# Kernel tuning notes

Measured on AMD Instinct MI355X. Metric: run time of the kernel, lower is better.

Reference implementation:

```python
import jax, jax.numpy as jnp
import numpy as np

EPS = 1e-5
K = 16  # neighbors

def bn(x, g, b):
    # BatchNorm in training mode: stats over all axes except the last (channel)
    ax = tuple(range(x.ndim - 1))
    m = x.mean(ax, keepdims=True)
    v = x.var(ax, keepdims=True)
    return g * (x - m) * jax.lax.rsqrt(v + EPS) + b

def setup_inputs() -> dict:
    key = jax.random.key(0)
    ks = jax.random.split(key, 12)
    B, N, M, C, D = 2, 16384, 4096, 32, 64
    H = D // 2
    p = lambda k, s: jax.random.normal(k, s, dtype=jnp.float32) * 0.1
    inp = {}
    inp["xyz"] = jax.random.normal(ks[0], (B, N, 3), dtype=jnp.float32)
    inp["feats"] = jax.random.normal(ks[1], (B, C, N), dtype=jnp.float32)
    inp["sample_idx"] = jax.random.randint(ks[2], (B, M), 0, N, dtype=jnp.int32)
    # RelativePosEncoder mlp: Conv2d(10, H, 1) + BN
    inp["W_pos"] = p(ks[3], (10, H)); inp["b_pos"] = jnp.zeros(H); inp["g_pos"] = jnp.ones(H); inp["be_pos"] = jnp.zeros(H)
    # feature_mlp: Conv2d(C, H, 1) + BN
    inp["W_feat"] = p(ks[4], (C, H)); inp["b_feat"] = jnp.zeros(H); inp["g_feat"] = jnp.ones(H); inp["be_feat"] = jnp.zeros(H)
    # attention score mlp: Conv2d(D, D, 1, bias=False)
    inp["W_score"] = p(ks[5], (D, D))
    # out_mlp: Conv1d(D, D, 1, bias=False) + BN
    inp["W_out"] = p(ks[6], (D, D)); inp["g_out"] = jnp.ones(D); inp["be_out"] = jnp.zeros(D)
    # LFA shortcut: Conv1d(C, D, 1, bias=False) + BN
    inp["W_sc1"] = p(ks[7], (C, D)); inp["g_sc1"] = jnp.ones(D); inp["be_sc1"] = jnp.zeros(D)
    # unit shortcut: Conv1d(C, D, 1, bias=False) + BN
    inp["W_sc2"] = p(ks[8], (C, D)); inp["g_sc2"] = jnp.ones(D); inp["be_sc2"] = jnp.zeros(D)
    return inp

def reference(xyz, feats, sample_idx,
              W_pos, b_pos, g_pos, be_pos,
              W_feat, b_feat, g_feat, be_feat,
              W_score,
              W_out, g_out, be_out,
              W_sc1, g_sc1, be_sc1,
              W_sc2, g_sc2, be_sc2):
    B, C, N = feats.shape
    featsT = jnp.transpose(feats, (0, 2, 1))                    # [B,N,C]
    xyz_ds = jnp.take_along_axis(xyz, sample_idx[:, :, None], axis=1)  # [B,M,3]
    # KNN: squared distances are monotone in cdist -> same topk indices
    d2 = jnp.sum((xyz_ds[:, :, None, :] - xyz[:, None, :, :]) ** 2, axis=-1)  # [B,M,N]
    _, knn_idx = jax.lax.top_k(-d2, K)                           # [B,M,K]
    gather = jax.vmap(lambda pts, idx: pts[idx])
    neigh_xyz = gather(xyz, knn_idx)                             # [B,M,K,3]
    neigh_feats = gather(featsT, knn_idx)                        # [B,M,K,C]
    center_feats = jnp.take_along_axis(featsT, sample_idx[:, :, None], axis=1)  # [B,M,C]
    # relative position encoding
    center = jnp.broadcast_to(xyz_ds[:, :, None, :], neigh_xyz.shape)
    rel = xyz_ds[:, :, None, :] - neigh_xyz                      # [B,M,K,3]
    dist = jnp.linalg.norm(rel, axis=-1, keepdims=True)          # [B,M,K,1]
    posf = jnp.concatenate([center, neigh_xyz, rel, dist], axis=-1)  # [B,M,K,10]
    pos_feats = jax.nn.relu(bn(posf @ W_pos + b_pos, g_pos, be_pos))       # [B,M,K,H]
    feat_feats = jax.nn.relu(bn(neigh_feats @ W_feat + b_feat, g_feat, be_feat))  # [B,M,K,H]
    combined = jnp.concatenate([feat_feats, pos_feats], axis=-1)  # [B,M,K,D]
    # attention pooling: softmax over the K (neighbor) axis
    scores = jax.nn.softmax(combined @ W_score, axis=2)
    pooled = jnp.sum(scores * combined, axis=2)                  # [B,M,D]
    out = jax.nn.relu(bn(pooled @ W_out, g_out, be_out))         # [B,M,D]
    sc1 = bn(jnp.mean(neigh_feats, axis=2) @ W_sc1, g_sc1, be_sc1)
    f_lfa = out + sc1
    f_sc = bn(center_feats @ W_sc2, g_sc2, be_sc2)
    y = jax.nn.relu(f_lfa + f_sc)                                # [B,M,D]
    return xyz_ds, jnp.transpose(y, (0, 2, 1)), sample_idx
```

## Files before the change

### kernel.cpp

```cpp
#include <hip/hip_runtime.h>
#include <math.h>

#define BB 2
#define NN 16384
#define MM 4096
#define C_IN 32
#define D_DIM 64
#define H_DIM 32
#define KNB 16
#define EPSV 1e-5f
#define FLT_BIG 3.0e38f
#define CAPK 128
#define NSPL 4
#define SPTS (NN / NSPL)

#define SPOS_SUM 0
#define SPOS_SQ 32
#define SFEAT_SUM 64
#define SFEAT_SQ 96
#define SSC1_SUM 128
#define SSC1_SQ 192
#define SSC2_SUM 256
#define SSC2_SQ 320
#define SOUT_SUM 384
#define SOUT_SQ 448
#define STATS_LEN 512
#define PA_W 384
#define PB_W 128
#define NBLK (BB * MM / 4)

__device__ __forceinline__ int clampi_r14(int v, int lo, int hi) {
    return v < lo ? lo : (v > hi ? hi : v);
}

__global__ __launch_bounds__(256) void prep_r14(const float* __restrict__ feats,
                                                const float* __restrict__ xyz,
                                                const int* __restrict__ sample_idx,
                                                float* __restrict__ featsT,
                                                float* __restrict__ xyz4,
                                                float* __restrict__ stats,
                                                float* __restrict__ out) {
    __shared__ float tile[C_IN][65];
    const int tid = threadIdx.x;
    const int b = blockIdx.x >> 8;
    const int n0 = (blockIdx.x & 255) * 64;
#pragma unroll
    for (int it = 0; it < 8; ++it) {
        int c = (tid >> 6) + 4 * it;
        int n = tid & 63;
        tile[c][n] = feats[((size_t)b * C_IN + c) * NN + n0 + n];
    }
    int e = blockIdx.x * 256 + tid;
    if (e < STATS_LEN) stats[e] = 0.f;
    if (e < BB * NN) {
        float x = xyz[e * 3 + 0], y = xyz[e * 3 + 1], z = xyz[e * 3 + 2];
        xyz4[e * 4 + 0] = x;
        xyz4[e * 4 + 1] = y;
        xyz4[e * 4 + 2] = z;
        xyz4[e * 4 + 3] = x * x + y * y + z * z;
    }
    if (e < BB * MM) {
        int bb2 = e >> 12;
        int sidx = clampi_r14(sample_idx[e], 0, NN - 1);
        const float* p = xyz + (size_t)(bb2 * NN + sidx) * 3;
        out[e * 3 + 0] = p[0];
        out[e * 3 + 1] = p[1];
        out[e * 3 + 2] = p[2];
        out[BB * MM * 3 + BB * D_DIM * MM + e] = (float)sample_idx[e];
    }
    __syncthreads();
#pragma unroll
    for (int it = 0; it < 8; ++it) {
        int c = tid & 31;
        int nn = (tid >> 5) + 8 * it;
        featsT[((size_t)b * NN + n0 + nn) * C_IN + c] = tile[c][nn];
    }
}

__device__ void knn_fullsplit_r14(const float* __restrict__ base4, int n0,
                                  float m2x, float m2y, float m2z, int lane,
                                  float* __restrict__ outd, int* __restrict__ outi) {
    float d2v[KNB]; int iv[KNB];
#pragma unroll
    for (int i = 0; i < KNB; i++) { d2v[i] = FLT_BIG; iv[i] = 0x7FFFFFFF; }
    float curmax = FLT_BIG; int amax = 0;
    for (int t = 0; t < SPTS / 64; ++t) {
        int n = n0 + lane + t * 64;
        const float4 p = *reinterpret_cast<const float4*>(base4 + (size_t)n * 4);
        float d2 = fmaf(p.x, m2x, p.w);
        d2 = fmaf(p.y, m2y, d2);
        d2 = fmaf(p.z, m2z, d2);
        if (d2 < curmax) {
#pragma unroll
            for (int i = 0; i < KNB; i++)
                if (i == amax) { d2v[i] = d2; iv[i] = n; }
            curmax = d2v[0]; amax = 0;
#pragma unroll
            for (int i = 1; i < KNB; i++)
                if (d2v[i] > curmax) { curmax = d2v[i]; amax = i; }
        }
    }
#pragma unroll
    for (int i = 0; i < KNB; i++) {
#pragma unroll
        for (int j = 0; j < KNB - 1; j++) {
            bool sw = (d2v[j] > d2v[j + 1]) ||
                      (d2v[j] == d2v[j + 1] && iv[j] > iv[j + 1]);
            if (sw) {
                float td = d2v[j]; d2v[j] = d2v[j + 1]; d2v[j + 1] = td;
                int   ti = iv[j];  iv[j]  = iv[j + 1];  iv[j + 1]  = ti;
            }
        }
    }
    float myd = FLT_BIG; int myidx = 0x7FFFFFFF;
#pragma unroll 1
    for (int r = 0; r < KNB; r++) {
        float cv = d2v[0]; int cid = iv[0]; int ml = lane;
#pragma unroll
        for (int off = 32; off > 0; off >>= 1) {
            float ov = __shfl_xor(cv, off);
            int   oid = __shfl_xor(cid, off);
            int   ol = __shfl_xor(ml, off);
            bool take = (ov < cv) || (ov == cv && oid < cid);
            cv = take ? ov : cv; cid = take ? oid : cid; ml = take ? ol : ml;
        }
        if (lane == r) { myd = cv; myidx = cid; }
        if (lane == ml) {
#pragma unroll
            for (int i = 0; i < KNB - 1; i++) { d2v[i] = d2v[i + 1]; iv[i] = iv[i + 1]; }
            d2v[KNB - 1] = FLT_BIG; iv[KNB - 1] = 0x7FFFFFFF;
        }
    }
    if (lane < KNB) { outd[lane] = myd; outi[lane] = myidx; }
}

__global__ __launch_bounds__(256) void knn_r14(const float* __restrict__ xyz4,
                                               const int* __restrict__ sample_idx,
                                               float* __restrict__ cand_d,
                                               int* __restrict__ cand_i) {
    __shared__ float bufd[16][CAPK];
    __shared__ int   bufi[16][CAPK];
    __shared__ int   cnt_lds[16];
    const int tid = threadIdx.x;
    const int w = tid >> 6, lane = tid & 63;
    const int split = blockIdx.x & (NSPL - 1);
    const int qgrp = blockIdx.x >> 2;
    const int qbase = qgrp * 16 + w * 4;
    const int b = qbase >> 12;
    const int n0 = split * SPTS;
    if (tid < 16) cnt_lds[tid] = 0;
    __syncthreads();
    const float* base4 = xyz4 + (size_t)b * NN * 4;
    const float4* p4 = reinterpret_cast<const float4*>(base4) + n0 + lane;

    float m2x[4], m2y[4], m2z[4], md[4], v16[4];
#pragma unroll
    for (int j = 0; j < 4; j++) {
        int s = clampi_r14(sample_idx[qbase + j], 0, NN - 1);
        m2x[j] = -2.f * base4[(size_t)s * 4 + 0];
        m2y[j] = -2.f * base4[(size_t)s * 4 + 1];
        m2z[j] = -2.f * base4[(size_t)s * 4 + 2];
        md[j] = FLT_BIG;
    }
#pragma unroll 8
    for (int it = 0; it < SPTS / 64; ++it) {
        const float4 p = p4[(size_t)it * 64];
#pragma unroll
        for (int j = 0; j < 4; j++) {
            float t = fmaf(p.x, m2x[j], p.w);
            t = fmaf(p.y, m2y[j], t);
            t = fmaf(p.z, m2z[j], t);
            md[j] = fminf(md[j], t);
        }
    }
#pragma unroll 1
    for (int j = 0; j < 4; j++) {
        unsigned fb = __float_as_uint(md[j]);
        unsigned key = (fb & 0x80000000u) ? ~fb : (fb | 0x80000000u);
        unsigned lo = 0u, hi = 0xFFFFFFFFu;
#pragma unroll 1
        for (int itb = 0; itb < 18; ++itb) {
            unsigned mid = lo + ((hi - lo) >> 1);
            unsigned long long bal = __ballot(key <= mid);
            int c = __popcll(bal);
            if (c >= KNB) hi = mid; else lo = mid + 1;
        }
        unsigned vb = (hi & 0x80000000u) ? (hi & 0x7FFFFFFFu) : ~hi;
        v16[j] = __uint_as_float(vb);
    }
#pragma unroll 4
    for (int it = 0; it < SPTS / 64; ++it) {
        const float4 p = p4[(size_t)it * 64];
        const int n = n0 + lane + it * 64;
#pragma unroll
        for (int j = 0; j < 4; j++) {
            float t = fmaf(p.x, m2x[j], p.w);
            t = fmaf(p.y, m2y[j], t);
            t = fmaf(p.z, m2z[j], t);
            if (t <= v16[j]) {
                int pos = atomicAdd(&cnt_lds[w * 4 + j], 1);
                if (pos < CAPK) { bufd[w * 4 + j][pos] = t; bufi[w * 4 + j][pos] = n; }
            }
        }
    }
    __threadfence_block();
#pragma unroll 1
    for (int j = 0; j < 4; j++) {
        const int qi = w * 4 + j;
        const int cnt = cnt_lds[qi];
        const int q = qbase + j;
        float* outd = cand_d + ((size_t)q * NSPL + split) * KNB;
        int*   outi = cand_i + ((size_t)q * NSPL + split) * KNB;
        if (cnt <= CAPK) {
#pragma unroll 1
            for (int half = 0; half < 2; ++half) {
                int i = lane + 64 * half;
                if (i < cnt) {
                    float di = bufd[qi][i]; int xi = bufi[qi][i];
                    int rank = 0;
                    for (int t = 0; t < cnt; ++t) {
                        float dt = bufd[qi][t]; int xt = bufi[qi][t];
                        rank += (dt < di || (dt == di && xt < xi)) ? 1 : 0;
                    }
                    if (rank < KNB) { outd[rank] = di; outi[rank] = xi; }
                }
            }
        } else {
            knn_fullsplit_r14(base4, n0, m2x[j], m2y[j], m2z[j], lane, outd, outi);
        }
    }
}

__device__ __forceinline__ void prebn_r14(const float (*posf)[12], const float (*nf)[C_IN],
                                          int k, int h,
                                          const float* __restrict__ W_pos, const float* __restrict__ b_pos,
                                          const float* __restrict__ W_feat, const float* __restrict__ b_feat,
                                          float* a_out, float* f_out) {
    float4 p0 = *reinterpret_cast<const float4*>(&posf[k][0]);
    float4 p1 = *reinterpret_cast<const float4*>(&posf[k][4]);
    float p8 = posf[k][8], p9 = posf[k][9];
    float a = b_pos[h];
    a += p0.x * W_pos[0 * H_DIM + h]; a += p0.y * W_pos[1 * H_DIM + h];
    a += p0.z * W_pos[2 * H_DIM + h]; a += p0.w * W_pos[3 * H_DIM + h];
    a += p1.x * W_pos[4 * H_DIM + h]; a += p1.y * W_pos[5 * H_DIM + h];
    a += p1.z * W_pos[6 * H_DIM + h]; a += p1.w * W_pos[7 * H_DIM + h];
    a += p8 * W_pos[8 * H_DIM + h];   a += p9 * W_pos[9 * H_DIM + h];
    float f = b_feat[h];
#pragma unroll
    for (int j4 = 0; j4 < C_IN / 4; ++j4) {
        float4 c = *reinterpret_cast<const float4*>(&nf[k][j4 * 4]);
        f += c.x * W_feat[(j4 * 4 + 0) * H_DIM + h];
        f += c.y * W_feat[(j4 * 4 + 1) * H_DIM + h];
        f += c.z * W_feat[(j4 * 4 + 2) * H_DIM + h];
        f += c.w * W_feat[(j4 * 4 + 3) * H_DIM + h];
    }
    *a_out = a; *f_out = f;
}

__global__ __launch_bounds__(256) void stageA_r14(const float* __restrict__ xyz4,
                                                  const int* __restrict__ sample_idx,
                                                  const float* __restrict__ featsT,
                                                  const float* __restrict__ cand_d,
                                                  const int* __restrict__ cand_i,
                                                  const float* __restrict__ W_pos, const float* __restrict__ b_pos,
                                                  const float* __restrict__ W_feat, const float* __restrict__ b_feat,
                                                  const float* __restrict__ W_sc1, const float* __restrict__ W_sc2,
                                                  float* __restrict__ combpre,
                                                  float* __restrict__ sc1_pre, float* __restrict__ sc2_pre,
                                                  float* __restrict__ partialsA) {
    __shared__ int   idxs[4][KNB];
    __shared__ float sd[4][64];
    __shared__ int   si[4][64];
    __shared__ __align__(16) float posf[4][KNB][12];
    __shared__ __align__(16) float nf[4][KNB][C_IN];
    __shared__ float meanf[4][C_IN];
    __shared__ float centerf[4][C_IN];
    __shared__ float posS[4][H_DIM], posQ[4][H_DIM], featS[4][H_DIM], featQ[4][H_DIM];
    __shared__ float s1S[4][D_DIM], s1Q[4][D_DIM], s2S[4][D_DIM], s2Q[4][D_DIM];
    const int tid = threadIdx.x;
    const int w = tid >> 6, lane = tid & 63;
    const int q = blockIdx.x * 4 + w;
    const int b = q >> 12;
    const int sidx = clampi_r14(sample_idx[q], 0, NN - 1);
    const float* base4 = xyz4 + (size_t)b * NN * 4;

    float d = cand_d[(size_t)q * 64 + lane];
    int   i = cand_i[(size_t)q * 64 + lane];
    float qx = base4[(size_t)sidx * 4 + 0];
    float qy = base4[(size_t)sidx * 4 + 1];
    float qz = base4[(size_t)sidx * 4 + 2];
    float cfv = 0.f;
    if (lane < C_IN) cfv = featsT[((size_t)b * NN + sidx) * C_IN + lane];

    {
        sd[w][lane] = d; si[w][lane] = i;
        __syncthreads();
        int rank = 0;
#pragma unroll
        for (int t = 0; t < 64; ++t) {
            float dt = sd[w][t]; int it = si[w][t];
            rank += (dt < d || (dt == d && it < i)) ? 1 : 0;
        }
        if (rank < KNB) idxs[w][rank] = i;
        if (lane < C_IN) centerf[w][lane] = cfv;
        __syncthreads();
    }

    if (lane < KNB) {
        int idx = clampi_r14(idxs[w][lane], 0, NN - 1);
        float nx = base4[(size_t)idx * 4 + 0];
        float ny = base4[(size_t)idx * 4 + 1];
        float nz = base4[(size_t)idx * 4 + 2];
        float rx = qx - nx, ry = qy - ny, rz = qz - nz;
        float dist = sqrtf(rx * rx + ry * ry + rz * rz);
        posf[w][lane][0] = qx; posf[w][lane][1] = qy; posf[w][lane][2] = qz;
        posf[w][lane][3] = nx; posf[w][lane][4] = ny; posf[w][lane][5] = nz;
        posf[w][lane][6] = rx; posf[w][lane][7] = ry; posf[w][lane][8] = rz;
        posf[w][lane][9] = dist; posf[w][lane][10] = 0.f; posf[w][lane][11] = 0.f;
    }
    __syncthreads();
    const float* fT = featsT + (size_t)b * NN * C_IN;
#pragma unroll
    for (int ii = 0; ii < 2; ++ii) {
        int e4 = lane + 64 * ii;
        int k = e4 >> 3, c4 = e4 & 7;
        const float4 v = *reinterpret_cast<const float4*>(fT + (size_t)idxs[w][k] * C_IN + c4 * 4);
        *reinterpret_cast<float4*>(&nf[w][k][c4 * 4]) = v;
    }
    __syncthreads();

    const int h = lane & 31;
    float sP = 0.f, qP = 0.f, sF = 0.f, qF = 0.f;
    float* cp = combpre + (size_t)q * (KNB * D_DIM);
#pragma unroll
    for (int i2 = 0; i2 < 8; i2++) {
        int k = ((lane + 64 * i2) >> 5);
        float a, f;
        prebn_r14(posf[w], nf[w], k, h, W_pos, b_pos, W_feat, b_feat, &a, &f);
        sP += a; qP += a * a;
        sF += f; qF += f * f;
        cp[k * D_DIM + h] = f;
        cp[k * D_DIM + H_DIM + h] = a;
    }
    sP += __shfl_xor(sP, 32); qP += __shfl_xor(qP, 32);
    sF += __shfl_xor(sF, 32); qF += __shfl_xor(qF, 32);
    if (lane < H_DIM) {
        posS[w][h] = sP; posQ[w][h] = qP; featS[w][h] = sF; featQ[w][h] = qF;
    }
    if (lane < C_IN) {
        float s = 0.f;
#pragma unroll
        for (int k = 0; k < KNB; k++) s += nf[w][k][lane];
        meanf[w][lane] = s * (1.f / (float)KNB);
    }
    __syncthreads();
    {
        float a = 0.f, c2 = 0.f;
#pragma unroll
        for (int j = 0; j < C_IN; j++) {
            a  += meanf[w][j]   * W_sc1[j * D_DIM + lane];
            c2 += centerf[w][j] * W_sc2[j * D_DIM + lane];
        }
        sc1_pre[(size_t)q * D_DIM + lane] = a;
        sc2_pre[(size_t)q * D_DIM + lane] = c2;
        s1S[w][lane] = a;  s1Q[w][lane] = a * a;
        s2S[w][lane] = c2; s2Q[w][lane] = c2 * c2;
    }
    __syncthreads();
    float* row = partialsA + (size_t)blockIdx.x * PA_W;
    if (tid < H_DIM) {
        row[SPOS_SUM + tid]  = posS[0][tid] + posS[1][tid] + posS[2][tid] + posS[3][tid];
        row[SPOS_SQ + tid]   = posQ[0][tid] + posQ[1][tid] + posQ[2][tid] + posQ[3][tid];
        row[SFEAT_SUM + tid] = featS[0][tid] + featS[1][tid] + featS[2][tid] + featS[3][tid];
        row[SFEAT_SQ + tid]  = featQ[0][tid] + featQ[1][tid] + featQ[2][tid] + featQ[3][tid];
    } else if (tid >= 64 && tid < 128) {
        int dd = tid - 64;
        row[SSC1_SUM + dd] = s1S[0][dd] + s1S[1][dd] + s1S[2][dd] + s1S[3][dd];
        row[SSC1_SQ + dd]  = s1Q[0][dd] + s1Q[1][dd] + s1Q[2][dd] + s1Q[3][dd];
    } else if (tid >= 128 && tid < 192) {
        int dd = tid - 128;
        row[SSC2_SUM + dd] = s2S[0][dd] + s2S[1][dd] + s2S[2][dd] + s2S[3][dd];
        row[SSC2_SQ + dd]  = s2Q[0][dd] + s2Q[1][dd] + s2Q[2][dd] + s2Q[3][dd];
    }
}

#define NRSPLIT 64
__global__ __launch_bounds__(256) void reduce_r14(const float* __restrict__ partials,
                                                  int rows, int width,
                                                  float* __restrict__ stats_out) {
    const int wchunks = (width + 255) / 256;
    const int wi = blockIdx.x % wchunks;
    const int pi = blockIdx.x / wchunks;
    const int c = wi * 256 + threadIdx.x;
    if (c >= width) return;
    const int per = rows / NRSPLIT;
    const int p0 = pi * per;
    float s = 0.f;
    for (int p = p0; p < p0 + per; ++p) s += partials[(size_t)p * width + c];
    atomicAdd(&stats_out[c], s);
}

__global__ __launch_bounds__(256) void stageB_r14(const float* __restrict__ combpre,
                                                  const float* __restrict__ g_pos, const float* __restrict__ be_pos,
                                                  const float* __restrict__ g_feat, const float* __restrict__ be_feat,
                                                  const float* __restrict__ W_score, const float* __restrict__ W_out,
                                                  const float* __restrict__ stats,
                                                  float* __restrict__ out_pre,
                                                  float* __restrict__ partialsB) {
    __shared__ __align__(16) float comb[4][KNB][D_DIM];
    __shared__ float scl[D_DIM], shf[D_DIM];
    __shared__ float pooled[4][D_DIM];
    __shared__ float oS[4][D_DIM], oQ[4][D_DIM];
    const int tid = threadIdx.x;
    const int w = tid >> 6, lane = tid & 63;
    const int q = blockIdx.x * 4 + w;

    if (tid < D_DIM) {
        const float inv1 = 1.f / (float)(BB * MM * KNB);
        float mean, var, g, bb;
        if (tid < H_DIM) {
            mean = stats[SFEAT_SUM + tid] * inv1;
            var  = fmaxf(stats[SFEAT_SQ + tid] * inv1 - mean * mean, 0.f);
            g = g_feat[tid]; bb = be_feat[tid];
        } else {
            int h = tid - H_DIM;
            mean = stats[SPOS_SUM + h] * inv1;
            var  = fmaxf(stats[SPOS_SQ + h] * inv1 - mean * mean, 0.f);
            g = g_pos[h]; bb = be_pos[h];
        }
        float s = g * rsqrtf(var + EPSV);
        scl[tid] = s;
        shf[tid] = bb - mean * s;
    }
    __syncthreads();

    const float4* src = reinterpret_cast<const float4*>(combpre + (size_t)blockIdx.x * 4 * KNB * D_DIM);
#pragma unroll
    for (int i = 0; i < 4; ++i) {
        int f = tid + 256 * i;
        int qloc = f >> 8;
        int k = (f >> 4) & 15;
        int j4 = f & 15;
        float4 v = src[f];
        int j = j4 * 4;
        v.x = fmaxf(v.x * scl[j + 0] + shf[j + 0], 0.f);
        v.y = fmaxf(v.y * scl[j + 1] + shf[j + 1], 0.f);
        v.z = fmaxf(v.z * scl[j + 2] + shf[j + 2], 0.f);
        v.w = fmaxf(v.w * scl[j + 3] + shf[j + 3], 0.f);
        *reinterpret_cast<float4*>(&comb[qloc][k][j]) = v;
    }
    __syncthreads();

    const int d = lane;
    float s[KNB];
#pragma unroll
    for (int k = 0; k < KNB; k++) s[k] = 0.f;
#pragma unroll 4
    for (int j4 = 0; j4 < D_DIM / 4; ++j4) {
        float w0 = W_score[(j4 * 4 + 0) * D_DIM + d];
        float w1 = W_score[(j4 * 4 + 1) * D_DIM + d];
        float w2 = W_score[(j4 * 4 + 2) * D_DIM + d];
        float w3 = W_score[(j4 * 4 + 3) * D_DIM + d];
#pragma unroll
        for (int k = 0; k < KNB; k++) {
            float4 cb = *reinterpret_cast<const float4*>(&comb[w][k][j4 * 4]);
            s[k] += cb.x * w0 + cb.y * w1 + cb.z * w2 + cb.w * w3;
        }
    }
    float mx = s[0];
#pragma unroll
    for (int k = 1; k < KNB; k++) mx = fmaxf(mx, s[k]);
    float sum = 0.f;
#pragma unroll
    for (int k = 0; k < KNB; k++) { s[k] = __expf(s[k] - mx); sum += s[k]; }
    float inv = 1.f / sum;
    float pv = 0.f;
#pragma unroll
    for (int k = 0; k < KNB; k++) pv += s[k] * inv * comb[w][k][d];
    pooled[w][d] = pv;
    __syncthreads();
    float o = 0.f;
#pragma unroll
    for (int dd = 0; dd < D_DIM; dd++) o += pooled[w][dd] * W_out[dd * D_DIM + d];
    out_pre[(size_t)q * D_DIM + d] = o;
    oS[w][d] = o; oQ[w][d] = o * o;
    __syncthreads();
    float* row = partialsB + (size_t)blockIdx.x * PB_W;
    if (tid < D_DIM) {
        row[tid] = oS[0][tid] + oS[1][tid] + oS[2][tid] + oS[3][tid];
    } else if (tid < 2 * D_DIM) {
        int dd = tid - D_DIM;
        row[D_DIM + dd] = oQ[0][dd] + oQ[1][dd] + oQ[2][dd] + oQ[3][dd];
    }
}

__global__ __launch_bounds__(256) void final_r14(const float* __restrict__ out_pre,
                                                 const float* __restrict__ sc1_pre,
                                                 const float* __restrict__ sc2_pre,
                                                 const float* __restrict__ stats,
                                                 const float* __restrict__ g_out, const float* __restrict__ be_out,
                                                 const float* __restrict__ g_sc1, const float* __restrict__ be_sc1,
                                                 const float* __restrict__ g_sc2, const float* __restrict__ be_sc2,
                                                 float* __restrict__ out) {
    __shared__ float yt[64][65];
    const int tid = threadIdx.x;
    const int blk = blockIdx.x;
    const int b = blk >> 6;
    const int m0 = (blk & 63) * 64;
    const int d = tid & 63;

    const float invn = 1.f / (float)(BB * MM);
    float mo = stats[SOUT_SUM + d] * invn;
    float vo = fmaxf(stats[SOUT_SQ + d] * invn - mo * mo, 0.f);
    float so = g_out[d] * rsqrtf(vo + EPSV);
    float oo = be_out[d] - mo * so;
    float m1 = stats[SSC1_SUM + d] * invn;
    float v1 = fmaxf(stats[SSC1_SQ + d] * invn - m1 * m1, 0.f);
    float s1 = g_sc1[d] * rsqrtf(v1 + EPSV);
    float o1 = be_sc1[d] - m1 * s1;
    float m2 = stats[SSC2_SUM + d] * invn;
    float v2 = fmaxf(stats[SSC2_SQ + d] * invn - m2 * m2, 0.f);
    float s2 = g_sc2[d] * rsqrtf(v2 + EPSV);
    float o2 = be_sc2[d] - m2 * s2;

#pragma unroll
    for (int p = 0; p < 16; p++) {
        int ml = (tid >> 6) + 4 * p;
        size_t q = (size_t)b * MM + m0 + ml;
        float x_out = fmaxf(out_pre[q * D_DIM + d] * so + oo, 0.f);
        float x1 = sc1_pre[q * D_DIM + d] * s1 + o1;
        float x2 = sc2_pre[q * D_DIM + d] * s2 + o2;
        yt[ml][d] = fmaxf(x_out + x1 + x2, 0.f);
    }
    __syncthreads();
#pragma unroll
    for (int p = 0; p < 16; p++) {
        int dr = (tid >> 6) + 4 * p;
        int mc = tid & 63;
        out[BB * MM * 3 + (size_t)b * (D_DIM * MM) + (size_t)dr * MM + m0 + mc] = yt[mc][dr];
    }
}

extern "C" void kernel_launch(void* const* d_in, const int* in_sizes, int n_in,
                              void* d_out, int out_size, void* d_ws, size_t ws_size,
                              hipStream_t stream) {
    const float* xyz        = (const float*)d_in[0];
    const float* feats      = (const float*)d_in[1];
    const int*   sample_idx = (const int*)d_in[2];
    const float* W_pos  = (const float*)d_in[3];
    const float* b_pos  = (const float*)d_in[4];
    const float* g_pos  = (const float*)d_in[5];
    const float* be_pos = (const float*)d_in[6];
    const float* W_feat  = (const float*)d_in[7];
    const float* b_feat  = (const float*)d_in[8];
    const float* g_feat  = (const float*)d_in[9];
    const float* be_feat = (const float*)d_in[10];
    const float* W_score = (const float*)d_in[11];
    const float* W_out  = (const float*)d_in[12];
    const float* g_out  = (const float*)d_in[13];
    const float* be_out = (const float*)d_in[14];
    const float* W_sc1  = (const float*)d_in[15];
    const float* g_sc1  = (const float*)d_in[16];
    const float* be_sc1 = (const float*)d_in[17];
    const float* W_sc2  = (const float*)d_in[18];
    const float* g_sc2  = (const float*)d_in[19];
    const float* be_sc2 = (const float*)d_in[20];

    float* out = (float*)d_out;
    float* ws = (float*)d_ws;

    float* featsT    = ws;
    float* xyz4      = featsT + 1048576;
    float* sc1_pre   = xyz4 + 131072;
    float* sc2_pre   = sc1_pre + 524288;
    float* out_pre   = sc2_pre + 524288;
    float* stats     = out_pre + 524288;
    float* partialsA = stats + STATS_LEN;
    float* partialsB = partialsA + NBLK * PA_W;
    float* cand_d    = partialsB + NBLK * PB_W;
    int*   cand_i    = (int*)(cand_d + (size_t)BB * MM * NSPL * KNB);
    float* combpre   = (float*)(cand_i + (size_t)BB * MM * NSPL * KNB);

    prep_r14<<<BB * (NN / 64), 256, 0, stream>>>(feats, xyz, sample_idx,
                                                 featsT, xyz4, stats, out);

    knn_r14<<<(BB * MM / 16) * NSPL, 256, 0, stream>>>(xyz4, sample_idx, cand_d, cand_i);

    stageA_r14<<<NBLK, 256, 0, stream>>>(xyz4, sample_idx, featsT, cand_d, cand_i,
                                         W_pos, b_pos, W_feat, b_feat, W_sc1, W_sc2,
                                         combpre, sc1_pre, sc2_pre, partialsA);
    reduce_r14<<<2 * NRSPLIT, 256, 0, stream>>>(partialsA, NBLK, PA_W, stats);

    stageB_r14<<<NBLK, 256, 0, stream>>>(combpre,
                                         g_pos, be_pos, g_feat, be_feat,
                                         W_score, W_out, stats, out_pre, partialsB);
    reduce_r14<<<1 * NRSPLIT, 256, 0, stream>>>(partialsB, NBLK, PB_W, stats + SOUT_SUM);

    final_r14<<<BB * (MM / 64), 256, 0, stream>>>(out_pre, sc1_pre, sc2_pre, stats,
                                                  g_out, be_out, g_sc1, be_sc1, g_sc2, be_sc2, out);
}
```

Baseline: 263.2 us.

## Compute a shared KNN distance bound per query in a separate pre-pass

```diff
diff --git a/kernel.cpp b/kernel.cpp
--- a/kernel.cpp
+++ b/kernel.cpp
@@ -13,6 +13,7 @@
 #define CAPK 128
 #define NSPL 4
 #define SPTS (NN / NSPL)
+#define BPTS 2048
 
 #define SPOS_SUM 0
 #define SPOS_SQ 32
@@ -29,11 +30,11 @@
 #define PB_W 128
 #define NBLK (BB * MM / 4)
 
-__device__ __forceinline__ int clampi_r14(int v, int lo, int hi) {
+__device__ __forceinline__ int clampi_r15(int v, int lo, int hi) {
     return v < lo ? lo : (v > hi ? hi : v);
 }
 
-__global__ __launch_bounds__(256) void prep_r14(const float* __restrict__ feats,
+__global__ __launch_bounds__(256) void prep_r15(const float* __restrict__ feats,
                                                 const float* __restrict__ xyz,
                                                 const int* __restrict__ sample_idx,
                                                 float* __restrict__ featsT,
@@ -61,7 +62,7 @@
     }
     if (e < BB * MM) {
         int bb2 = e >> 12;
-        int sidx = clampi_r14(sample_idx[e], 0, NN - 1);
+        int sidx = clampi_r15(sample_idx[e], 0, NN - 1);
         const float* p = xyz + (size_t)(bb2 * NN + sidx) * 3;
         out[e * 3 + 0] = p[0];
         out[e * 3 + 1] = p[1];
@@ -77,7 +78,66 @@
     }
 }
 
-__device__ void knn_fullsplit_r14(const float* __restrict__ base4, int n0,
+__global__ __launch_bounds__(256) void knnbound_r15(const float* __restrict__ xyz4,
+                                                    const int* __restrict__ sample_idx,
+                                                    float* __restrict__ bound,
+                                                    float* __restrict__ cand_d,
+                                                    int* __restrict__ cand_i) {
+    const int tid = threadIdx.x;
+    const int w = tid >> 6, lane = tid & 63;
+    const int qbase = blockIdx.x * 16 + w * 4;
+    const int b = qbase >> 12;
+    const float* base4 = xyz4 + (size_t)b * NN * 4;
+    const float4* p4 = reinterpret_cast<const float4*>(base4) + lane;
+
+    {
+        const int q0 = blockIdx.x * 16;
+#pragma unroll
+        for (int i = 0; i < 4; ++i) {
+            int s = tid + 256 * i;
+            cand_d[(size_t)q0 * 64 + s] = FLT_BIG;
+            cand_i[(size_t)q0 * 64 + s] = 0x7FFFFFFF;
+        }
+    }
+
+    float m2x[4], m2y[4], m2z[4], md[4];
+#pragma unroll
+    for (int j = 0; j < 4; j++) {
+        int s = clampi_r15(sample_idx[qbase + j], 0, NN - 1);
+        m2x[j] = -2.f * base4[(size_t)s * 4 + 0];
+        m2y[j] = -2.f * base4[(size_t)s * 4 + 1];
+        m2z[j] = -2.f * base4[(size_t)s * 4 + 2];
+        md[j] = FLT_BIG;
+    }
+#pragma unroll 8
+    for (int it = 0; it < BPTS / 64; ++it) {
+        const float4 p = p4[(size_t)it * 64];
+#pragma unroll
+        for (int j = 0; j < 4; j++) {
+            float t = fmaf(p.x, m2x[j], p.w);
+            t = fmaf(p.y, m2y[j], t);
+            t = fmaf(p.z, m2z[j], t);
+            md[j] = fminf(md[j], t);
+        }
+    }
+#pragma unroll 1
+    for (int j = 0; j < 4; j++) {
+        unsigned fb = __float_as_uint(md[j]);
+        unsigned key = (fb & 0x80000000u) ? ~fb : (fb | 0x80000000u);
+        unsigned lo = 0u, hi = 0xFFFFFFFFu;
+#pragma unroll 1
+        for (int itb = 0; itb < 18; ++itb) {
+            unsigned mid = lo + ((hi - lo) >> 1);
+            unsigned long long bal = __ballot(key <= mid);
+            int c = __popcll(bal);
+            if (c >= KNB) hi = mid; else lo = mid + 1;
+        }
+        unsigned vb = (hi & 0x80000000u) ? (hi & 0x7FFFFFFFu) : ~hi;
+        if (lane == 0) bound[qbase + j] = __uint_as_float(vb);
+    }
+}
+
+__device__ void knn_fullsplit_r15(const float* __restrict__ base4, int n0,
                                   float m2x, float m2y, float m2z, int lane,
                                   float* __restrict__ outd, int* __restrict__ outi) {
     float d2v[KNB]; int iv[KNB];
@@ -134,8 +194,9 @@
     if (lane < KNB) { outd[lane] = myd; outi[lane] = myidx; }
 }
 
-__global__ __launch_bounds__(256) void knn_r14(const float* __restrict__ xyz4,
+__global__ __launch_bounds__(256) void knn_r15(const float* __restrict__ xyz4,
                                                const int* __restrict__ sample_idx,
+                                               const float* __restrict__ bound,
                                                float* __restrict__ cand_d,
                                                int* __restrict__ cand_i) {
     __shared__ float bufd[16][CAPK];
@@ -153,42 +214,16 @@
     const float* base4 = xyz4 + (size_t)b * NN * 4;
     const float4* p4 = reinterpret_cast<const float4*>(base4) + n0 + lane;
 
-    float m2x[4], m2y[4], m2z[4], md[4], v16[4];
+    float m2x[4], m2y[4], m2z[4], v16[4];
 #pragma unroll
     for (int j = 0; j < 4; j++) {
-        int s = clampi_r14(sample_idx[qbase + j], 0, NN - 1);
+        int s = clampi_r15(sample_idx[qbase + j], 0, NN - 1);
         m2x[j] = -2.f * base4[(size_t)s * 4 + 0];
         m2y[j] = -2.f * base4[(size_t)s * 4 + 1];
         m2z[j] = -2.f * base4[(size_t)s * 4 + 2];
-        md[j] = FLT_BIG;
+        v16[j] = bound[qbase + j];
     }
 #pragma unroll 8
-    for (int it = 0; it < SPTS / 64; ++it) {
-        const float4 p = p4[(size_t)it * 64];
-#pragma unroll
-        for (int j = 0; j < 4; j++) {
-            float t = fmaf(p.x, m2x[j], p.w);
-            t = fmaf(p.y, m2y[j], t);
-            t = fmaf(p.z, m2z[j], t);
-            md[j] = fminf(md[j], t);
-        }
-    }
-#pragma unroll 1
-    for (int j = 0; j < 4; j++) {
-        unsigned fb = __float_as_uint(md[j]);
-        unsigned key = (fb & 0x80000000u) ? ~fb : (fb | 0x80000000u);
-        unsigned lo = 0u, hi = 0xFFFFFFFFu;
-#pragma unroll 1
-        for (int itb = 0; itb < 18; ++itb) {
-            unsigned mid = lo + ((hi - lo) >> 1);
-            unsigned long long bal = __ballot(key <= mid);
-            int c = __popcll(bal);
-            if (c >= KNB) hi = mid; else lo = mid + 1;
-        }
-        unsigned vb = (hi & 0x80000000u) ? (hi & 0x7FFFFFFFu) : ~hi;
-        v16[j] = __uint_as_float(vb);
-    }
-#pragma unroll 4
     for (int it = 0; it < SPTS / 64; ++it) {
         const float4 p = p4[(size_t)it * 64];
         const int n = n0 + lane + it * 64;
@@ -226,12 +261,12 @@
                 }
             }
         } else {
-            knn_fullsplit_r14(base4, n0, m2x[j], m2y[j], m2z[j], lane, outd, outi);
-        }
-    }
-}
-
-__device__ __forceinline__ void prebn_r14(const float (*posf)[12], const float (*nf)[C_IN],
+            knn_fullsplit_r15(base4, n0, m2x[j], m2y[j], m2z[j], lane, outd, outi);
+        }
+    }
+}
+
+__device__ __forceinline__ void prebn_r15(const float (*posf)[12], const float (*nf)[C_IN],
                                           int k, int h,
                                           const float* __restrict__ W_pos, const float* __restrict__ b_pos,
                                           const float* __restrict__ W_feat, const float* __restrict__ b_feat,
@@ -257,7 +292,7 @@
     *a_out = a; *f_out = f;
 }
 
-__global__ __launch_bounds__(256) void stageA_r14(const float* __restrict__ xyz4,
+__global__ __launch_bounds__(256) void stageA_r15(const float* __restrict__ xyz4,
                                                   const int* __restrict__ sample_idx,
                                                   const float* __restrict__ featsT,
                                                   const float* __restrict__ cand_d,
@@ -281,7 +316,7 @@
     const int w = tid >> 6, lane = tid & 63;
     const int q = blockIdx.x * 4 + w;
     const int b = q >> 12;
-    const int sidx = clampi_r14(sample_idx[q], 0, NN - 1);
+    const int sidx = clampi_r15(sample_idx[q], 0, NN - 1);
     const float* base4 = xyz4 + (size_t)b * NN * 4;
 
     float d = cand_d[(size_t)q * 64 + lane];
@@ -307,7 +342,7 @@
     }
 
     if (lane < KNB) {
-        int idx = clampi_r14(idxs[w][lane], 0, NN - 1);
+        int idx = clampi_r15(idxs[w][lane], 0, NN - 1);
         float nx = base4[(size_t)idx * 4 + 0];
         float ny = base4[(size_t)idx * 4 + 1];
         float nz = base4[(size_t)idx * 4 + 2];
@@ -336,7 +371,7 @@
     for (int i2 = 0; i2 < 8; i2++) {
         int k = ((lane + 64 * i2) >> 5);
         float a, f;
-        prebn_r14(posf[w], nf[w], k, h, W_pos, b_pos, W_feat, b_feat, &a, &f);
+        prebn_r15(posf[w], nf[w], k, h, W_pos, b_pos, W_feat, b_feat, &a, &f);
         sP += a; qP += a * a;
         sF += f; qF += f * f;
         cp[k * D_DIM + h] = f;
@@ -385,7 +420,7 @@
 }
 
 #define NRSPLIT 64
-__global__ __launch_bounds__(256) void reduce_r14(const float* __restrict__ partials,
+__global__ __launch_bounds__(256) void reduce_r15(const float* __restrict__ partials,
                                                   int rows, int width,
                                                   float* __restrict__ stats_out) {
     const int wchunks = (width + 255) / 256;
@@ -400,7 +435,7 @@
     atomicAdd(&stats_out[c], s);
 }
 
-__global__ __launch_bounds__(256) void stageB_r14(const float* __restrict__ combpre,
+__global__ __launch_bounds__(256) void stageB_r15(const float* __restrict__ combpre,
                                                   const float* __restrict__ g_pos, const float* __restrict__ be_pos,
                                                   const float* __restrict__ g_feat, const float* __restrict__ be_feat,
                                                   const float* __restrict__ W_score, const float* __restrict__ W_out,
@@ -494,7 +529,7 @@
     }
 }
 
-__global__ __launch_bounds__(256) void final_r14(const float* __restrict__ out_pre,
+__global__ __launch_bounds__(256) void final_r15(const float* __restrict__ out_pre,
                                                  const float* __restrict__ sc1_pre,
                                                  const float* __restrict__ sc2_pre,
                                                  const float* __restrict__ stats,
@@ -579,23 +614,26 @@
     float* partialsB = partialsA + NBLK * PA_W;
     float* cand_d    = partialsB + NBLK * PB_W;
     int*   cand_i    = (int*)(cand_d + (size_t)BB * MM * NSPL * KNB);
-    float* combpre   = (float*)(cand_i + (size_t)BB * MM * NSPL * KNB);
-
-    prep_r14<<<BB * (NN / 64), 256, 0, stream>>>(feats, xyz, sample_idx,
+    float* boundbuf  = (float*)(cand_i + (size_t)BB * MM * NSPL * KNB);
+    float* combpre   = boundbuf + BB * MM;
+
+    prep_r15<<<BB * (NN / 64), 256, 0, stream>>>(feats, xyz, sample_idx,
                                                  featsT, xyz4, stats, out);
 
-    knn_r14<<<(BB * MM / 16) * NSPL, 256, 0, stream>>>(xyz4, sample_idx, cand_d, cand_i);
-
-    stageA_r14<<<NBLK, 256, 0, stream>>>(xyz4, sample_idx, featsT, cand_d, cand_i,
+    knnbound_r15<<<BB * MM / 16, 256, 0, stream>>>(xyz4, sample_idx, boundbuf, cand_d, cand_i);
+
+    knn_r15<<<(BB * MM / 16) * NSPL, 256, 0, stream>>>(xyz4, sample_idx, boundbuf, cand_d, cand_i);
+
+    stageA_r15<<<NBLK, 256, 0, stream>>>(xyz4, sample_idx, featsT, cand_d, cand_i,
                                          W_pos, b_pos, W_feat, b_feat, W_sc1, W_sc2,
                                          combpre, sc1_pre, sc2_pre, partialsA);
-    reduce_r14<<<2 * NRSPLIT, 256, 0, stream>>>(partialsA, NBLK, PA_W, stats);
-
-    stageB_r14<<<NBLK, 256, 0, stream>>>(combpre,
+    reduce_r15<<<2 * NRSPLIT, 256, 0, stream>>>(partialsA, NBLK, PA_W, stats);
+
+    stageB_r15<<<NBLK, 256, 0, stream>>>(combpre,
                                          g_pos, be_pos, g_feat, be_feat,
                                          W_score, W_out, stats, out_pre, partialsB);
-    reduce_r14<<<1 * NRSPLIT, 256, 0, stream>>>(partialsB, NBLK, PB_W, stats + SOUT_SUM);
-
-    final_r14<<<BB * (MM / 64), 256, 0, stream>>>(out_pre, sc1_pre, sc2_pre, stats,
+    reduce_r15<<<1 * NRSPLIT, 256, 0, stream>>>(partialsB, NBLK, PB_W, stats + SOUT_SUM);
+
+    final_r15<<<BB * (MM / 64), 256, 0, stream>>>(out_pre, sc1_pre, sc2_pre, stats,
                                                   g_out, be_out, g_sc1, be_sc1, g_sc2, be_sc2, out);
 }
```

Result: slower. 297.6 us (+13.1%).

## Fuse BN stat reductions into stage kernels via bucketed atomics and last-block finish

Applied to the files above, without the earlier changes.

```diff
diff --git a/kernel.cpp b/kernel.cpp
--- a/kernel.cpp
+++ b/kernel.cpp
@@ -27,18 +27,19 @@
 #define STATS_LEN 512
 #define PA_W 384
 #define PB_W 128
+#define NBKT 64
 #define NBLK (BB * MM / 4)
 
-__device__ __forceinline__ int clampi_r14(int v, int lo, int hi) {
+__device__ __forceinline__ int clampi_r16(int v, int lo, int hi) {
     return v < lo ? lo : (v > hi ? hi : v);
 }
 
-__global__ __launch_bounds__(256) void prep_r14(const float* __restrict__ feats,
+__global__ __launch_bounds__(256) void prep_r16(const float* __restrict__ feats,
                                                 const float* __restrict__ xyz,
                                                 const int* __restrict__ sample_idx,
                                                 float* __restrict__ featsT,
                                                 float* __restrict__ xyz4,
-                                                float* __restrict__ stats,
+                                                float* __restrict__ statszero,
                                                 float* __restrict__ out) {
     __shared__ float tile[C_IN][65];
     const int tid = threadIdx.x;
@@ -51,7 +52,7 @@
         tile[c][n] = feats[((size_t)b * C_IN + c) * NN + n0 + n];
     }
     int e = blockIdx.x * 256 + tid;
-    if (e < STATS_LEN) stats[e] = 0.f;
+    if (e < STATS_LEN + NBKT * PA_W + NBKT * PB_W + 2) statszero[e] = 0.f;
     if (e < BB * NN) {
         float x = xyz[e * 3 + 0], y = xyz[e * 3 + 1], z = xyz[e * 3 + 2];
         xyz4[e * 4 + 0] = x;
@@ -61,7 +62,7 @@
     }
     if (e < BB * MM) {
         int bb2 = e >> 12;
-        int sidx = clampi_r14(sample_idx[e], 0, NN - 1);
+        int sidx = clampi_r16(sample_idx[e], 0, NN - 1);
         const float* p = xyz + (size_t)(bb2 * NN + sidx) * 3;
         out[e * 3 + 0] = p[0];
         out[e * 3 + 1] = p[1];
@@ -77,7 +78,7 @@
     }
 }
 
-__device__ void knn_fullsplit_r14(const float* __restrict__ base4, int n0,
+__device__ void knn_fullsplit_r16(const float* __restrict__ base4, int n0,
                                   float m2x, float m2y, float m2z, int lane,
                                   float* __restrict__ outd, int* __restrict__ outi) {
     float d2v[KNB]; int iv[KNB];
@@ -134,7 +135,7 @@
     if (lane < KNB) { outd[lane] = myd; outi[lane] = myidx; }
 }
 
-__global__ __launch_bounds__(256) void knn_r14(const float* __restrict__ xyz4,
+__global__ __launch_bounds__(256) void knn_r16(const float* __restrict__ xyz4,
                                                const int* __restrict__ sample_idx,
                                                float* __restrict__ cand_d,
                                                int* __restrict__ cand_i) {
@@ -156,7 +157,7 @@
     float m2x[4], m2y[4], m2z[4], md[4], v16[4];
 #pragma unroll
     for (int j = 0; j < 4; j++) {
-        int s = clampi_r14(sample_idx[qbase + j], 0, NN - 1);
+        int s = clampi_r16(sample_idx[qbase + j], 0, NN - 1);
         m2x[j] = -2.f * base4[(size_t)s * 4 + 0];
         m2y[j] = -2.f * base4[(size_t)s * 4 + 1];
         m2z[j] = -2.f * base4[(size_t)s * 4 + 2];
@@ -226,12 +227,12 @@
                 }
             }
         } else {
-            knn_fullsplit_r14(base4, n0, m2x[j], m2y[j], m2z[j], lane, outd, outi);
-        }
-    }
-}
-
-__device__ __forceinline__ void prebn_r14(const float (*posf)[12], const float (*nf)[C_IN],
+            knn_fullsplit_r16(base4, n0, m2x[j], m2y[j], m2z[j], lane, outd, outi);
+        }
+    }
+}
+
+__device__ __forceinline__ void prebn_r16(const float (*posf)[12], const float (*nf)[C_IN],
                                           int k, int h,
                                           const float* __restrict__ W_pos, const float* __restrict__ b_pos,
                                           const float* __restrict__ W_feat, const float* __restrict__ b_feat,
@@ -257,7 +258,7 @@
     *a_out = a; *f_out = f;
 }
 
-__global__ __launch_bounds__(256) void stageA_r14(const float* __restrict__ xyz4,
+__global__ __launch_bounds__(256) void stageA_r16(const float* __restrict__ xyz4,
                                                   const int* __restrict__ sample_idx,
                                                   const float* __restrict__ featsT,
                                                   const float* __restrict__ cand_d,
@@ -267,7 +268,9 @@
                                                   const float* __restrict__ W_sc1, const float* __restrict__ W_sc2,
                                                   float* __restrict__ combpre,
                                                   float* __restrict__ sc1_pre, float* __restrict__ sc2_pre,
-                                                  float* __restrict__ partialsA) {
+                                                  float* __restrict__ stats,
+                                                  float* __restrict__ stats64A,
+                                                  int* __restrict__ cntA) {
     __shared__ int   idxs[4][KNB];
     __shared__ float sd[4][64];
     __shared__ int   si[4][64];
@@ -277,11 +280,12 @@
     __shared__ float centerf[4][C_IN];
     __shared__ float posS[4][H_DIM], posQ[4][H_DIM], featS[4][H_DIM], featQ[4][H_DIM];
     __shared__ float s1S[4][D_DIM], s1Q[4][D_DIM], s2S[4][D_DIM], s2Q[4][D_DIM];
+    __shared__ int islast;
     const int tid = threadIdx.x;
     const int w = tid >> 6, lane = tid & 63;
     const int q = blockIdx.x * 4 + w;
     const int b = q >> 12;
-    const int sidx = clampi_r14(sample_idx[q], 0, NN - 1);
+    const int sidx = clampi_r16(sample_idx[q], 0, NN - 1);
     const float* base4 = xyz4 + (size_t)b * NN * 4;
 
     float d = cand_d[(size_t)q * 64 + lane];
@@ -307,7 +311,7 @@
     }
 
     if (lane < KNB) {
-        int idx = clampi_r14(idxs[w][lane], 0, NN - 1);
+        int idx = clampi_r16(idxs[w][lane], 0, NN - 1);
         float nx = base4[(size_t)idx * 4 + 0];
         float ny = base4[(size_t)idx * 4 + 1];
         float nz = base4[(size_t)idx * 4 + 2];
@@ -336,7 +340,7 @@
     for (int i2 = 0; i2 < 8; i2++) {
         int k = ((lane + 64 * i2) >> 5);
         float a, f;
-        prebn_r14(posf[w], nf[w], k, h, W_pos, b_pos, W_feat, b_feat, &a, &f);
+        prebn_r16(posf[w], nf[w], k, h, W_pos, b_pos, W_feat, b_feat, &a, &f);
         sP += a; qP += a * a;
         sF += f; qF += f * f;
         cp[k * D_DIM + h] = f;
@@ -367,50 +371,47 @@
         s2S[w][lane] = c2; s2Q[w][lane] = c2 * c2;
     }
     __syncthreads();
-    float* row = partialsA + (size_t)blockIdx.x * PA_W;
+    float* rowA = stats64A + (size_t)(blockIdx.x & (NBKT - 1)) * PA_W;
     if (tid < H_DIM) {
-        row[SPOS_SUM + tid]  = posS[0][tid] + posS[1][tid] + posS[2][tid] + posS[3][tid];
-        row[SPOS_SQ + tid]   = posQ[0][tid] + posQ[1][tid] + posQ[2][tid] + posQ[3][tid];
-        row[SFEAT_SUM + tid] = featS[0][tid] + featS[1][tid] + featS[2][tid] + featS[3][tid];
-        row[SFEAT_SQ + tid]  = featQ[0][tid] + featQ[1][tid] + featQ[2][tid] + featQ[3][tid];
-    } else if (tid >= 64 && tid < 128) {
+        atomicAdd(&rowA[SPOS_SUM + tid],  posS[0][tid] + posS[1][tid] + posS[2][tid] + posS[3][tid]);
+        atomicAdd(&rowA[SPOS_SQ + tid],   posQ[0][tid] + posQ[1][tid] + posQ[2][tid] + posQ[3][tid]);
+        atomicAdd(&rowA[SFEAT_SUM + tid], featS[0][tid] + featS[1][tid] + featS[2][tid] + featS[3][tid]);
+        atomicAdd(&rowA[SFEAT_SQ + tid],  featQ[0][tid] + featQ[1][tid] + featQ[2][tid] + featQ[3][tid]);
+    } else if (tid < 128) {
         int dd = tid - 64;
-        row[SSC1_SUM + dd] = s1S[0][dd] + s1S[1][dd] + s1S[2][dd] + s1S[3][dd];
-        row[SSC1_SQ + dd]  = s1Q[0][dd] + s1Q[1][dd] + s1Q[2][dd] + s1Q[3][dd];
-    } else if (tid >= 128 && tid < 192) {
+        atomicAdd(&rowA[SSC1_SUM + dd], s1S[0][dd] + s1S[1][dd] + s1S[2][dd] + s1S[3][dd]);
+        atomicAdd(&rowA[SSC1_SQ + dd],  s1Q[0][dd] + s1Q[1][dd] + s1Q[2][dd] + s1Q[3][dd]);
+    } else if (tid < 192) {
         int dd = tid - 128;
-        row[SSC2_SUM + dd] = s2S[0][dd] + s2S[1][dd] + s2S[2][dd] + s2S[3][dd];
-        row[SSC2_SQ + dd]  = s2Q[0][dd] + s2Q[1][dd] + s2Q[2][dd] + s2Q[3][dd];
-    }
-}
-
-#define NRSPLIT 64
-__global__ __launch_bounds__(256) void reduce_r14(const float* __restrict__ partials,
-                                                  int rows, int width,
-                                                  float* __restrict__ stats_out) {
-    const int wchunks = (width + 255) / 256;
-    const int wi = blockIdx.x % wchunks;
-    const int pi = blockIdx.x / wchunks;
-    const int c = wi * 256 + threadIdx.x;
-    if (c >= width) return;
-    const int per = rows / NRSPLIT;
-    const int p0 = pi * per;
-    float s = 0.f;
-    for (int p = p0; p < p0 + per; ++p) s += partials[(size_t)p * width + c];
-    atomicAdd(&stats_out[c], s);
-}
-
-__global__ __launch_bounds__(256) void stageB_r14(const float* __restrict__ combpre,
+        atomicAdd(&rowA[SSC2_SUM + dd], s2S[0][dd] + s2S[1][dd] + s2S[2][dd] + s2S[3][dd]);
+        atomicAdd(&rowA[SSC2_SQ + dd],  s2Q[0][dd] + s2Q[1][dd] + s2Q[2][dd] + s2Q[3][dd]);
+    }
+    __threadfence();
+    if (tid == 0) islast = (atomicAdd(cntA, 1) == NBLK - 1);
+    __syncthreads();
+    if (islast) {
+        __threadfence();
+        for (int c = tid; c < PA_W; c += 256) {
+            float s = 0.f;
+            for (int r = 0; r < NBKT; ++r) s += stats64A[(size_t)r * PA_W + c];
+            stats[c] = s;
+        }
+    }
+}
+
+__global__ __launch_bounds__(256) void stageB_r16(const float* __restrict__ combpre,
                                                   const float* __restrict__ g_pos, const float* __restrict__ be_pos,
                                                   const float* __restrict__ g_feat, const float* __restrict__ be_feat,
                                                   const float* __restrict__ W_score, const float* __restrict__ W_out,
-                                                  const float* __restrict__ stats,
+                                                  float* __restrict__ stats,
                                                   float* __restrict__ out_pre,
-                                                  float* __restrict__ partialsB) {
+                                                  float* __restrict__ stats64B,
+                                                  int* __restrict__ cntB) {
     __shared__ __align__(16) float comb[4][KNB][D_DIM];
     __shared__ float scl[D_DIM], shf[D_DIM];
     __shared__ float pooled[4][D_DIM];
     __shared__ float oS[4][D_DIM], oQ[4][D_DIM];
+    __shared__ int islast;
     const int tid = threadIdx.x;
     const int w = tid >> 6, lane = tid & 63;
     const int q = blockIdx.x * 4 + w;
@@ -485,16 +486,27 @@
     out_pre[(size_t)q * D_DIM + d] = o;
     oS[w][d] = o; oQ[w][d] = o * o;
     __syncthreads();
-    float* row = partialsB + (size_t)blockIdx.x * PB_W;
+    float* rowB = stats64B + (size_t)(blockIdx.x & (NBKT - 1)) * PB_W;
     if (tid < D_DIM) {
-        row[tid] = oS[0][tid] + oS[1][tid] + oS[2][tid] + oS[3][tid];
+        atomicAdd(&rowB[tid], oS[0][tid] + oS[1][tid] + oS[2][tid] + oS[3][tid]);
     } else if (tid < 2 * D_DIM) {
         int dd = tid - D_DIM;
-        row[D_DIM + dd] = oQ[0][dd] + oQ[1][dd] + oQ[2][dd] + oQ[3][dd];
-    }
-}
-
-__global__ __launch_bounds__(256) void final_r14(const float* __restrict__ out_pre,
+        atomicAdd(&rowB[D_DIM + dd], oQ[0][dd] + oQ[1][dd] + oQ[2][dd] + oQ[3][dd]);
+    }
+    __threadfence();
+    if (tid == 0) islast = (atomicAdd(cntB, 1) == NBLK - 1);
+    __syncthreads();
+    if (islast) {
+        __threadfence();
+        if (tid < PB_W) {
+            float ssum = 0.f;
+            for (int r = 0; r < NBKT; ++r) ssum += stats64B[(size_t)r * PB_W + tid];
+            stats[SOUT_SUM + tid] = ssum;
+        }
+    }
+}
+
+__global__ __launch_bounds__(256) void final_r16(const float* __restrict__ out_pre,
                                                  const float* __restrict__ sc1_pre,
                                                  const float* __restrict__ sc2_pre,
                                                  const float* __restrict__ stats,
@@ -569,33 +581,34 @@
     float* out = (float*)d_out;
     float* ws = (float*)d_ws;
 
-    float* featsT    = ws;
-    float* xyz4      = featsT + 1048576;
-    float* sc1_pre   = xyz4 + 131072;
-    float* sc2_pre   = sc1_pre + 524288;
-    float* out_pre   = sc2_pre + 524288;
-    float* stats     = out_pre + 524288;
-    float* partialsA = stats + STATS_LEN;
-    float* partialsB = partialsA + NBLK * PA_W;
-    float* cand_d    = partialsB + NBLK * PB_W;
-    int*   cand_i    = (int*)(cand_d + (size_t)BB * MM * NSPL * KNB);
-    float* combpre   = (float*)(cand_i + (size_t)BB * MM * NSPL * KNB);
-
-    prep_r14<<<BB * (NN / 64), 256, 0, stream>>>(feats, xyz, sample_idx,
+    float* featsT   = ws;
+    float* xyz4     = featsT + 1048576;
+    float* sc1_pre  = xyz4 + 131072;
+    float* sc2_pre  = sc1_pre + 524288;
+    float* out_pre  = sc2_pre + 524288;
+    float* stats    = out_pre + 524288;
+    float* stats64A = stats + STATS_LEN;
+    float* stats64B = stats64A + NBKT * PA_W;
+    int*   counters = (int*)(stats64B + NBKT * PB_W);
+    float* cand_d   = (float*)(counters + 2);
+    int*   cand_i   = (int*)(cand_d + (size_t)BB * MM * NSPL * KNB);
+    float* combpre  = (float*)(cand_i + (size_t)BB * MM * NSPL * KNB);
+
+    prep_r16<<<BB * (NN / 64), 256, 0, stream>>>(feats, xyz, sample_idx,
                                                  featsT, xyz4, stats, out);
 
-    knn_r14<<<(BB * MM / 16) * NSPL, 256, 0, stream>>>(xyz4, sample_idx, cand_d, cand_i);
-
-    stageA_r14<<<NBLK, 256, 0, stream>>>(xyz4, sample_idx, featsT, cand_d, cand_i,
+    knn_r16<<<(BB * MM / 16) * NSPL, 256, 0, stream>>>(xyz4, sample_idx, cand_d, cand_i);
+
+    stageA_r16<<<NBLK, 256, 0, stream>>>(xyz4, sample_idx, featsT, cand_d, cand_i,
                                          W_pos, b_pos, W_feat, b_feat, W_sc1, W_sc2,
-                                         combpre, sc1_pre, sc2_pre, partialsA);
-    reduce_r14<<<2 * NRSPLIT, 256, 0, stream>>>(partialsA, NBLK, PA_W, stats);
-
-    stageB_r14<<<NBLK, 256, 0, stream>>>(combpre,
+                                         combpre, sc1_pre, sc2_pre,
+                                         stats, stats64A, counters + 0);
+
+    stageB_r16<<<NBLK, 256, 0, stream>>>(combpre,
                                          g_pos, be_pos, g_feat, be_feat,
-                                         W_score, W_out, stats, out_pre, partialsB);
-    reduce_r14<<<1 * NRSPLIT, 256, 0, stream>>>(partialsB, NBLK, PB_W, stats + SOUT_SUM);
-
-    final_r14<<<BB * (MM / 64), 256, 0, stream>>>(out_pre, sc1_pre, sc2_pre, stats,
+                                         W_score, W_out, stats, out_pre,
+                                         stats64B, counters + 1);
+
+    final_r16<<<BB * (MM / 64), 256, 0, stream>>>(out_pre, sc1_pre, sc2_pre, stats,
                                                   g_out, be_out, g_sc1, be_sc1, g_sc2, be_sc2, out);
 }
```

Result: slower. 584.7 us (+122.2%).
